# Kernel optimization log

Hardware: AMD Instinct MI355X
Metric: run time of the kernel (lower is better)

## Reference

```python
import jax, jax.numpy as jnp
import numpy as np

N = 50000
F_DIM = 128
H_DIM = 128
E = 800000


def setup_inputs() -> dict:
    key = jax.random.key(0)
    ks = jax.random.split(key, 8)
    x = jax.random.normal(ks[0], (N, F_DIM), dtype=jnp.float32)
    edge_weight = jax.random.uniform(ks[1], (E,), dtype=jnp.float32)
    src = jax.random.randint(ks[2], (E,), 0, N)
    dst = jax.random.randint(ks[3], (E,), 0, N)
    edge_index = jnp.stack([src, dst]).astype(jnp.int64)
    sc = 1.0 / np.sqrt(F_DIM)
    W1 = jax.random.normal(ks[4], (F_DIM, H_DIM), dtype=jnp.float32) * sc
    W2 = jax.random.normal(ks[5], (H_DIM, H_DIM), dtype=jnp.float32) * sc
    Wfc = jax.random.normal(ks[6], (H_DIM, F_DIM), dtype=jnp.float32) * sc
    b1 = jnp.zeros((H_DIM,), jnp.float32)
    b2 = jnp.zeros((H_DIM,), jnp.float32)
    bfc = jnp.zeros((F_DIM,), jnp.float32)
    return {"x": x, "edge_weight": edge_weight, "W1": W1, "b1": b1,
            "W2": W2, "b2": b2, "Wfc": Wfc, "bfc": bfc,
            "edge_index": edge_index}


def _gcn_norm(src, dst, edge_weight, num_nodes):
    # PyG gcn_norm: add self-loops (weight 1), symmetric D^-1/2 A D^-1/2
    loop = jnp.arange(num_nodes, dtype=src.dtype)
    src2 = jnp.concatenate([src, loop])
    dst2 = jnp.concatenate([dst, loop])
    w2 = jnp.concatenate([edge_weight, jnp.ones((num_nodes,), edge_weight.dtype)])
    deg = jax.ops.segment_sum(w2, dst2, num_segments=num_nodes)
    dinv = jnp.where(deg > 0, jax.lax.rsqrt(jnp.where(deg > 0, deg, 1.0)), 0.0)
    norm = dinv[src2] * w2 * dinv[dst2]
    return src2, dst2, norm


def _gcn_conv(x, W, b, src, dst, norm, num_nodes):
    h = x @ W                              # [N, out]
    msg = norm[:, None] * h[src]           # gather + scale, [E+N, out]
    agg = jax.ops.segment_sum(msg, dst, num_segments=num_nodes)
    return agg + b


def reference(x, edge_weight, W1, b1, W2, b2, Wfc, bfc, edge_index):
    src, dst = edge_index[0], edge_index[1]
    src2, dst2, norm = _gcn_norm(src, dst, edge_weight, N)
    h = jax.nn.relu(_gcn_conv(x, W1, b1, src2, dst2, norm, N))
    h = jax.nn.relu(_gcn_conv(h, W2, b2, src2, dst2, norm, N))
    return h @ Wfc + bfc
```

## Files before the change

kernel.cpp:

```cpp
#include <hip/hip_runtime.h>
#include <hip/hip_fp16.h>


typedef unsigned long long u64;
typedef _Float16 f16x8 __attribute__((ext_vector_type(8)));
typedef float f32x4 __attribute__((ext_vector_type(4)));

__global__ __launch_bounds__(256) void k_init(u64* packed, int n) {
    int i = blockIdx.x * 256 + threadIdx.x;
    if (i < n) packed[i] = 0ULL;
}

__global__ __launch_bounds__(256) void k_edge_deg(const int* __restrict__ dst,
                                                  const float* __restrict__ w,
                                                  u64* __restrict__ packed,
                                                  unsigned int* __restrict__ rank, int E) {
    int e = blockIdx.x * 256 + threadIdx.x;
    if (e < E) {
        int d = dst[e];
        u64 add = (1ULL << 40) | (u64)(w[e] * 16777216.0f);
        u64 old = atomicAdd(&packed[d], add);
        rank[e] = (unsigned int)(old >> 40);
    }
}

__global__ __launch_bounds__(256) void k_part(const u64* __restrict__ packed,
                                              float* __restrict__ dinv,
                                              int* __restrict__ bsum, int n) {
    __shared__ int red[256];
    int t = threadIdx.x;
    int i = blockIdx.x * 256 + t;
    int c = 0;
    if (i < n) {
        u64 p = packed[i];
        c = (int)(p >> 40);
        float degsum = (float)(p & ((1ULL << 40) - 1)) * (1.0f / 16777216.0f);
        dinv[i] = rsqrtf(1.0f + degsum);
    }
    red[t] = c;
    __syncthreads();
#pragma unroll
    for (int off = 128; off > 0; off >>= 1) {
        if (t < off) red[t] += red[t + off];
        __syncthreads();
    }
    if (t == 0) bsum[blockIdx.x] = red[0];
}

__global__ __launch_bounds__(256) void k_scan_bsums(int* bsum, int nb) {
    __shared__ int s[256];
    int t = threadIdx.x;
    s[t] = (t < nb) ? bsum[t] : 0;
    __syncthreads();
#pragma unroll
    for (int off = 1; off < 256; off <<= 1) {
        int u = (t >= off) ? s[t - off] : 0;
        __syncthreads();
        s[t] += u;
        __syncthreads();
    }
    if (t < nb) bsum[t] = (t == 0) ? 0 : s[t - 1];
}

__global__ __launch_bounds__(256) void k_rowptr(const u64* __restrict__ packed,
                                                const int* __restrict__ bsum,
                                                int* __restrict__ rowptr, int n) {
    __shared__ int s[256];
    int t = threadIdx.x;
    int i = blockIdx.x * 256 + t;
    int c = (i < n) ? (int)(packed[i] >> 40) : 0;
    s[t] = c;
    __syncthreads();
#pragma unroll
    for (int off = 1; off < 256; off <<= 1) {
        int u = (t >= off) ? s[t - off] : 0;
        __syncthreads();
        s[t] += u;
        __syncthreads();
    }
    int excl = bsum[blockIdx.x] + s[t] - c;
    if (i < n) rowptr[i] = excl;
    if (i == n - 1) rowptr[n] = excl + c;
}

__global__ __launch_bounds__(256) void k_scatter(const int* __restrict__ src,
                                                 const int* __restrict__ dst,
                                                 const float* __restrict__ w,
                                                 const unsigned int* __restrict__ rank,
                                                 const float* __restrict__ dinv,
                                                 const int* __restrict__ rowptr,
                                                 int* __restrict__ col,
                                                 float* __restrict__ val, int E) {
    int e = blockIdx.x * 256 + threadIdx.x;
    if (e < E) {
        int s = src[e], d = dst[e];
        int p = rowptr[d] + (int)rank[e];
        col[p] = s;
        val[p] = dinv[s] * w[e] * dinv[d];
    }
}

__global__ __launch_bounds__(256) void k_prepw(const float* __restrict__ W1,
                                               const float* __restrict__ W2,
                                               const float* __restrict__ Wfc,
                                               __half* __restrict__ Wt) {
    int i = blockIdx.x * 256 + threadIdx.x;
    if (i >= 3 * 16384) return;
    int w = i >> 14, r = i & 16383;
    int nn = r >> 7, kk = r & 127;
    const float* W = (w == 0) ? W1 : (w == 1) ? W2 : Wfc;
    Wt[i] = __float2half(W[kk * 128 + nn]);
}

template <bool IN_FP32, bool OUT_HALF>
__global__ __launch_bounds__(256) void k_gemm_mfma(const void* __restrict__ Xv,
                                                   const __half* __restrict__ Wt,
                                                   const float* __restrict__ bias,
                                                   void* __restrict__ Yv, int n) {
    __shared__ __align__(16) _Float16 Ws[128][136];
    int t = threadIdx.x;
    for (int i = t; i < 2048; i += 256) {
        int r = i >> 4, c8 = (i & 15) << 3;
        *(f16x8*)&Ws[r][c8] = *(const f16x8*)((const _Float16*)Wt + r * 128 + c8);
    }
    __syncthreads();

    int wave = t >> 6, lane = t & 63;
    int quad = lane >> 4, fcol = lane & 15;
    int rowbase = blockIdx.x * 64 + wave * 16;
    int arow = rowbase + fcol;

    f16x8 a[4];
#pragma unroll
    for (int c = 0; c < 4; c++) {
        int k0 = c * 32 + quad * 8;
        if (arow < n) {
            if (IN_FP32) {
                const float* p = (const float*)Xv + (size_t)arow * 128 + k0;
#pragma unroll
                for (int j = 0; j < 8; j++) a[c][j] = (_Float16)p[j];
            } else {
                a[c] = *(const f16x8*)((const _Float16*)Xv + (size_t)arow * 128 + k0);
            }
        } else {
            f16x8 z = {0, 0, 0, 0, 0, 0, 0, 0};
            a[c] = z;
        }
    }

    f32x4 acc[8];
#pragma unroll
    for (int c = 0; c < 8; c++) acc[c] = (f32x4){0.f, 0.f, 0.f, 0.f};

#pragma unroll
    for (int kc = 0; kc < 4; kc++) {
        int k0 = kc * 32 + quad * 8;
#pragma unroll
        for (int ct = 0; ct < 8; ct++) {
            f16x8 b = *(const f16x8*)&Ws[ct * 16 + fcol][k0];
            acc[ct] = __builtin_amdgcn_mfma_f32_16x16x32_f16(a[kc], b, acc[ct], 0, 0, 0);
        }
    }

#pragma unroll
    for (int reg = 0; reg < 4; reg++) {
        int gr = rowbase + quad * 4 + reg;
        if (gr < n) {
            if (OUT_HALF) {
                __half* Y = (__half*)Yv;
#pragma unroll
                for (int ct = 0; ct < 8; ct++)
                    Y[(size_t)gr * 128 + ct * 16 + fcol] = __float2half(acc[ct][reg]);
            } else {
                float* Y = (float*)Yv;
#pragma unroll
                for (int ct = 0; ct < 8; ct++)
                    Y[(size_t)gr * 128 + ct * 16 + fcol] = acc[ct][reg] + bias[ct * 16 + fcol];
            }
        }
    }
}

__global__ __launch_bounds__(256) void k_agg(const __half* __restrict__ H,
                                             const int* __restrict__ rowptr,
                                             const int* __restrict__ col,
                                             const float* __restrict__ val,
                                             const float* __restrict__ dinv,
                                             const float* __restrict__ bias,
                                             __half* __restrict__ out, int n) {
    int wid = (blockIdx.x * 256 + threadIdx.x) >> 6;
    int lane = threadIdx.x & 63;
    if (wid >= n) return;
    int i = __builtin_amdgcn_readfirstlane(wid);
    float di = dinv[i];
    float2 h0 = __half22float2(((const __half2*)(H + (size_t)i * 128))[lane]);
    float w0 = di * di;
    float ax = w0 * h0.x, ay = w0 * h0.y;
    int e0 = rowptr[i], e1 = rowptr[i + 1];

    for (int base = e0; base < e1; base += 64) {
        int cnt = min(64, e1 - base);
        int myc = 0; float myv = 0.f;
        if (lane < cnt) { myc = col[base + lane]; myv = val[base + lane]; }
        int j = 0;
        for (; j + 8 <= cnt; j += 8) {
            float2 h[8];
            float v[8];
#pragma unroll
            for (int u = 0; u < 8; u++) {
                int s = __shfl(myc, j + u);
                v[u] = __shfl(myv, j + u);
                h[u] = __half22float2(((const __half2*)(H + (size_t)s * 128))[lane]);
            }
#pragma unroll
            for (int u = 0; u < 8; u++) {
                ax = fmaf(v[u], h[u].x, ax);
                ay = fmaf(v[u], h[u].y, ay);
            }
        }
        for (; j < cnt; j++) {
            int s = __shfl(myc, j);
            float v = __shfl(myv, j);
            float2 h = __half22float2(((const __half2*)(H + (size_t)s * 128))[lane]);
            ax = fmaf(v, h.x, ax);
            ay = fmaf(v, h.y, ay);
        }
    }
    float2 b = ((const float2*)bias)[lane];
    ax = fmaxf(ax + b.x, 0.f);
    ay = fmaxf(ay + b.y, 0.f);
    ((__half2*)(out + (size_t)i * 128))[lane] = __floats2half2_rn(ax, ay);
}

extern "C" void kernel_launch(void* const* d_in, const int* in_sizes, int n_in,
                              void* d_out, int out_size, void* d_ws, size_t ws_size,
                              hipStream_t stream) {
    const float* x   = (const float*)d_in[0];
    const float* ew  = (const float*)d_in[1];
    const float* W1  = (const float*)d_in[2];
    const float* b1  = (const float*)d_in[3];
    const float* W2  = (const float*)d_in[4];
    const float* b2  = (const float*)d_in[5];
    const float* Wfc = (const float*)d_in[6];
    const float* bfc = (const float*)d_in[7];
    const int* eidx  = (const int*)d_in[8];

    const int E = in_sizes[1];
    const int N = in_sizes[0] / 128;
    const int* src = eidx;
    const int* dst = eidx + E;

    char* ws = (char*)d_ws;
    size_t off = 0;
    auto alloc = [&](size_t bytes) -> void* {
        void* p = ws + off;
        off = (off + bytes + 255) & ~(size_t)255;
        return p;
    };
    int nb = (N + 255) / 256;
    int eb = (E + 255) / 256;
    int gb = (N + 63) / 64;
    int ab = (N * 64 + 255) / 256;
    int Npad = N + 64;

    u64*   packed = (u64*)alloc((size_t)N * 8);
    float* dinv   = (float*)alloc((size_t)N * 4);
    int*   rowptr = (int*)alloc((size_t)(N + 1) * 4);
    int*   bsum   = (int*)alloc((size_t)nb * 4);
    unsigned int* rank = (unsigned int*)alloc((size_t)E * 4);
    int*   col    = (int*)alloc((size_t)E * 4);
    float* val    = (float*)alloc((size_t)E * 4);
    __half* Wt    = (__half*)alloc((size_t)3 * 16384 * 2);
    __half* bufH  = (__half*)alloc((size_t)Npad * 128 * 2);
    __half* bufA  = (__half*)alloc((size_t)Npad * 128 * 2);

    k_init<<<nb, 256, 0, stream>>>(packed, N);
    k_edge_deg<<<eb, 256, 0, stream>>>(dst, ew, packed, rank, E);
    k_part<<<nb, 256, 0, stream>>>(packed, dinv, bsum, N);
    k_scan_bsums<<<1, 256, 0, stream>>>(bsum, nb);
    k_rowptr<<<nb, 256, 0, stream>>>(packed, bsum, rowptr, N);
    k_scatter<<<eb, 256, 0, stream>>>(src, dst, ew, rank, dinv, rowptr, col, val, E);
    k_prepw<<<192, 256, 0, stream>>>(W1, W2, Wfc, Wt);

    k_gemm_mfma<true, true><<<gb, 256, 0, stream>>>(x, Wt, nullptr, bufH, N);
    k_agg<<<ab, 256, 0, stream>>>(bufH, rowptr, col, val, dinv, b1, bufA, N);
    k_gemm_mfma<false, true><<<gb, 256, 0, stream>>>(bufA, Wt + 16384, nullptr, bufH, N);
    k_agg<<<ab, 256, 0, stream>>>(bufH, rowptr, col, val, dinv, b2, bufA, N);
    k_gemm_mfma<false, false><<<gb, 256, 0, stream>>>(bufA, Wt + 2 * 16384, bfc, d_out, N);
}
```

Measured before the change: 259.0 us.

## Fuse setup kernels, co-launch degree with first GEMM, pack CSR pairs

Merges the init and weight-prep kernels into one launch. The degree-atomic pass and the first GEMM now share a single grid, so independent work runs concurrently. The separate col/val arrays become one int2 pairs array, so k_agg does one load per edge, and its inner gather loop is unrolled to 16 with a masked 8-wide tail. The GEMM reads weights straight from global memory instead of staging them in LDS, which drops the barrier but may add L1/L2 traffic.

```diff
diff --git a/kernel.cpp b/kernel.cpp
--- a/kernel.cpp
+++ b/kernel.cpp
@@ -6,22 +6,110 @@
 typedef _Float16 f16x8 __attribute__((ext_vector_type(8)));
 typedef float f32x4 __attribute__((ext_vector_type(4)));
 
-__global__ __launch_bounds__(256) void k_init(u64* packed, int n) {
+__global__ __launch_bounds__(256) void k_pre(u64* packed, int n,
+                                             const float* __restrict__ W1,
+                                             const float* __restrict__ W2,
+                                             const float* __restrict__ Wfc,
+                                             __half* __restrict__ Wt) {
     int i = blockIdx.x * 256 + threadIdx.x;
     if (i < n) packed[i] = 0ULL;
-}
-
-__global__ __launch_bounds__(256) void k_edge_deg(const int* __restrict__ dst,
-                                                  const float* __restrict__ w,
-                                                  u64* __restrict__ packed,
-                                                  unsigned int* __restrict__ rank, int E) {
-    int e = blockIdx.x * 256 + threadIdx.x;
-    if (e < E) {
-        int d = dst[e];
-        u64 add = (1ULL << 40) | (u64)(w[e] * 16777216.0f);
-        u64 old = atomicAdd(&packed[d], add);
-        rank[e] = (unsigned int)(old >> 40);
-    }
+    if (i < 3 * 16384) {
+        int w = i >> 14, r = i & 16383;
+        int nn = r >> 7, kk = r & 127;
+        const float* W = (w == 0) ? W1 : (w == 1) ? W2 : Wfc;
+        Wt[i] = __float2half(W[kk * 128 + nn]);
+    }
+}
+
+template <bool IN_FP32, bool OUT_HALF>
+__device__ __forceinline__ void gemm_body(int bid, int t, const void* __restrict__ Xv,
+                                          const _Float16* __restrict__ Wt,
+                                          const float* __restrict__ bias,
+                                          void* __restrict__ Yv, int n) {
+    int wave = t >> 6, lane = t & 63;
+    int quad = lane >> 4, fcol = lane & 15;
+    int rowbase = bid * 64 + wave * 16;
+    int arow = rowbase + fcol;
+
+    f16x8 a[4];
+#pragma unroll
+    for (int c = 0; c < 4; c++) {
+        int k0 = c * 32 + quad * 8;
+        if (arow < n) {
+            if (IN_FP32) {
+                const float* p = (const float*)Xv + (size_t)arow * 128 + k0;
+#pragma unroll
+                for (int j = 0; j < 8; j++) a[c][j] = (_Float16)p[j];
+            } else {
+                a[c] = *(const f16x8*)((const _Float16*)Xv + (size_t)arow * 128 + k0);
+            }
+        } else {
+            f16x8 z = {0, 0, 0, 0, 0, 0, 0, 0};
+            a[c] = z;
+        }
+    }
+
+    f32x4 acc[8];
+#pragma unroll
+    for (int c = 0; c < 8; c++) acc[c] = (f32x4){0.f, 0.f, 0.f, 0.f};
+
+#pragma unroll
+    for (int kc = 0; kc < 4; kc++) {
+        int k0 = kc * 32 + quad * 8;
+#pragma unroll
+        for (int ct = 0; ct < 8; ct++) {
+            f16x8 b = *(const f16x8*)(Wt + (size_t)(ct * 16 + fcol) * 128 + k0);
+            acc[ct] = __builtin_amdgcn_mfma_f32_16x16x32_f16(a[kc], b, acc[ct], 0, 0, 0);
+        }
+    }
+
+#pragma unroll
+    for (int reg = 0; reg < 4; reg++) {
+        int gr = rowbase + quad * 4 + reg;
+        if (gr < n) {
+            if (OUT_HALF) {
+                __half* Y = (__half*)Yv;
+#pragma unroll
+                for (int ct = 0; ct < 8; ct++)
+                    Y[(size_t)gr * 128 + ct * 16 + fcol] = __float2half(acc[ct][reg]);
+            } else {
+                float* Y = (float*)Yv;
+#pragma unroll
+                for (int ct = 0; ct < 8; ct++)
+                    Y[(size_t)gr * 128 + ct * 16 + fcol] = acc[ct][reg] + bias[ct * 16 + fcol];
+            }
+        }
+    }
+}
+
+__global__ __launch_bounds__(256) void k_deg_gemm1(const int* __restrict__ dst,
+                                                   const float* __restrict__ ew,
+                                                   u64* __restrict__ packed,
+                                                   unsigned int* __restrict__ rank,
+                                                   int E, int eb,
+                                                   const float* __restrict__ x,
+                                                   const _Float16* __restrict__ Wt,
+                                                   __half* __restrict__ bufH, int n) {
+    int t = threadIdx.x;
+    if ((int)blockIdx.x < eb) {
+        int e = blockIdx.x * 256 + t;
+        if (e < E) {
+            int d = dst[e];
+            u64 add = (1ULL << 40) | (u64)(ew[e] * 16777216.0f);
+            u64 old = atomicAdd(&packed[d], add);
+            rank[e] = (unsigned int)(old >> 40);
+        }
+    } else {
+        gemm_body<true, true>(blockIdx.x - eb, t, x, Wt, nullptr, bufH, n);
+    }
+}
+
+template <bool IN_FP32, bool OUT_HALF>
+__global__ __launch_bounds__(256) void k_gemm(const void* __restrict__ Xv,
+                                              const _Float16* __restrict__ Wt,
+                                              const float* __restrict__ bias,
+                                              void* __restrict__ Yv, int n) {
+    gemm_body<IN_FP32, OUT_HALF>(blockIdx.x, threadIdx.x, Xv, Wt, bias, Yv, n);
 }
 
 __global__ __launch_bounds__(256) void k_part(const u64* __restrict__ packed,
@@ -89,102 +177,18 @@
                                                  const unsigned int* __restrict__ rank,
                                                  const float* __restrict__ dinv,
                                                  const int* __restrict__ rowptr,
-                                                 int* __restrict__ col,
-                                                 float* __restrict__ val, int E) {
+                                                 int2* __restrict__ pairs, int E) {
     int e = blockIdx.x * 256 + threadIdx.x;
     if (e < E) {
         int s = src[e], d = dst[e];
         int p = rowptr[d] + (int)rank[e];
-        col[p] = s;
-        val[p] = dinv[s] * w[e] * dinv[d];
-    }
-}
-
-__global__ __launch_bounds__(256) void k_prepw(const float* __restrict__ W1,
-                                               const float* __restrict__ W2,
-                                               const float* __restrict__ Wfc,
-                                               __half* __restrict__ Wt) {
-    int i = blockIdx.x * 256 + threadIdx.x;
-    if (i >= 3 * 16384) return;
-    int w = i >> 14, r = i & 16383;
-    int nn = r >> 7, kk = r & 127;
-    const float* W = (w == 0) ? W1 : (w == 1) ? W2 : Wfc;
-    Wt[i] = __float2half(W[kk * 128 + nn]);
-}
-
-template <bool IN_FP32, bool OUT_HALF>
-__global__ __launch_bounds__(256) void k_gemm_mfma(const void* __restrict__ Xv,
-                                                   const __half* __restrict__ Wt,
-                                                   const float* __restrict__ bias,
-                                                   void* __restrict__ Yv, int n) {
-    __shared__ __align__(16) _Float16 Ws[128][136];
-    int t = threadIdx.x;
-    for (int i = t; i < 2048; i += 256) {
-        int r = i >> 4, c8 = (i & 15) << 3;
-        *(f16x8*)&Ws[r][c8] = *(const f16x8*)((const _Float16*)Wt + r * 128 + c8);
-    }
-    __syncthreads();
-
-    int wave = t >> 6, lane = t & 63;
-    int quad = lane >> 4, fcol = lane & 15;
-    int rowbase = blockIdx.x * 64 + wave * 16;
-    int arow = rowbase + fcol;
-
-    f16x8 a[4];
-#pragma unroll
-    for (int c = 0; c < 4; c++) {
-        int k0 = c * 32 + quad * 8;
-        if (arow < n) {
-            if (IN_FP32) {
-                const float* p = (const float*)Xv + (size_t)arow * 128 + k0;
-#pragma unroll
-                for (int j = 0; j < 8; j++) a[c][j] = (_Float16)p[j];
-            } else {
-                a[c] = *(const f16x8*)((const _Float16*)Xv + (size_t)arow * 128 + k0);
-            }
-        } else {
-            f16x8 z = {0, 0, 0, 0, 0, 0, 0, 0};
-            a[c] = z;
-        }
-    }
-
-    f32x4 acc[8];
-#pragma unroll
-    for (int c = 0; c < 8; c++) acc[c] = (f32x4){0.f, 0.f, 0.f, 0.f};
-
-#pragma unroll
-    for (int kc = 0; kc < 4; kc++) {
-        int k0 = kc * 32 + quad * 8;
-#pragma unroll
-        for (int ct = 0; ct < 8; ct++) {
-            f16x8 b = *(const f16x8*)&Ws[ct * 16 + fcol][k0];
-            acc[ct] = __builtin_amdgcn_mfma_f32_16x16x32_f16(a[kc], b, acc[ct], 0, 0, 0);
-        }
-    }
-
-#pragma unroll
-    for (int reg = 0; reg < 4; reg++) {
-        int gr = rowbase + quad * 4 + reg;
-        if (gr < n) {
-            if (OUT_HALF) {
-                __half* Y = (__half*)Yv;
-#pragma unroll
-                for (int ct = 0; ct < 8; ct++)
-                    Y[(size_t)gr * 128 + ct * 16 + fcol] = __float2half(acc[ct][reg]);
-            } else {
-                float* Y = (float*)Yv;
-#pragma unroll
-                for (int ct = 0; ct < 8; ct++)
-                    Y[(size_t)gr * 128 + ct * 16 + fcol] = acc[ct][reg] + bias[ct * 16 + fcol];
-            }
-        }
+        pairs[p] = make_int2(s, __float_as_int(dinv[s] * w[e] * dinv[d]));
     }
 }
 
 __global__ __launch_bounds__(256) void k_agg(const __half* __restrict__ H,
                                              const int* __restrict__ rowptr,
-                                             const int* __restrict__ col,
-                                             const float* __restrict__ val,
+                                             const int2* __restrict__ pairs,
                                              const float* __restrict__ dinv,
                                              const float* __restrict__ bias,
                                              __half* __restrict__ out, int n) {
@@ -200,16 +204,38 @@
 
     for (int base = e0; base < e1; base += 64) {
         int cnt = min(64, e1 - base);
-        int myc = 0; float myv = 0.f;
-        if (lane < cnt) { myc = col[base + lane]; myv = val[base + lane]; }
+        int mys = 0; float myv = 0.f;
+        if (lane < cnt) {
+            int2 pr = pairs[base + lane];
+            mys = pr.x;
+            myv = __int_as_float(pr.y);
+        }
         int j = 0;
-        for (; j + 8 <= cnt; j += 8) {
+        for (; j + 16 <= cnt; j += 16) {
+            float2 h[16];
+            float v[16];
+#pragma unroll
+            for (int u = 0; u < 16; u++) {
+                int s = __shfl(mys, j + u);
+                v[u] = __shfl(myv, j + u);
+                h[u] = __half22float2(((const __half2*)(H + (size_t)s * 128))[lane]);
+            }
+#pragma unroll
+            for (int u = 0; u < 16; u++) {
+                ax = fmaf(v[u], h[u].x, ax);
+                ay = fmaf(v[u], h[u].y, ay);
+            }
+        }
+        for (; j < cnt; j += 8) {
             float2 h[8];
             float v[8];
 #pragma unroll
             for (int u = 0; u < 8; u++) {
-                int s = __shfl(myc, j + u);
-                v[u] = __shfl(myv, j + u);
+                int idx = j + u;
+                int lsrc = min(idx, cnt - 1);
+                int s = __shfl(mys, lsrc);
+                float tv = __shfl(myv, lsrc);
+                v[u] = (idx < cnt) ? tv : 0.f;
                 h[u] = __half22float2(((const __half2*)(H + (size_t)s * 128))[lane]);
             }
 #pragma unroll
@@ -217,13 +243,6 @@
                 ax = fmaf(v[u], h[u].x, ax);
                 ay = fmaf(v[u], h[u].y, ay);
             }
-        }
-        for (; j < cnt; j++) {
-            int s = __shfl(myc, j);
-            float v = __shfl(myv, j);
-            float2 h = __half22float2(((const __half2*)(H + (size_t)s * 128))[lane]);
-            ax = fmaf(v, h.x, ax);
-            ay = fmaf(v, h.y, ay);
         }
     }
     float2 b = ((const float2*)bias)[lane];
@@ -261,6 +280,7 @@
     int eb = (E + 255) / 256;
     int gb = (N + 63) / 64;
     int ab = (N * 64 + 255) / 256;
+    int pb = (max(N, 3 * 16384) + 255) / 256;
     int Npad = N + 64;
 
     u64*   packed = (u64*)alloc((size_t)N * 8);
@@ -268,23 +288,25 @@
     int*   rowptr = (int*)alloc((size_t)(N + 1) * 4);
     int*   bsum   = (int*)alloc((size_t)nb * 4);
     unsigned int* rank = (unsigned int*)alloc((size_t)E * 4);
-    int*   col    = (int*)alloc((size_t)E * 4);
-    float* val    = (float*)alloc((size_t)E * 4);
+    int2*  pairs  = (int2*)alloc((size_t)E * 8);
     __half* Wt    = (__half*)alloc((size_t)3 * 16384 * 2);
     __half* bufH  = (__half*)alloc((size_t)Npad * 128 * 2);
     __half* bufA  = (__half*)alloc((size_t)Npad * 128 * 2);
 
-    k_init<<<nb, 256, 0, stream>>>(packed, N);
-    k_edge_deg<<<eb, 256, 0, stream>>>(dst, ew, packed, rank, E);
+    const _Float16* Wt1 = (const _Float16*)Wt;
+    const _Float16* Wt2 = Wt1 + 16384;
+    const _Float16* Wt3 = Wt1 + 2 * 16384;
+
+    k_pre<<<pb, 256, 0, stream>>>(packed, N, W1, W2, Wfc, Wt);
+    k_deg_gemm1<<<eb + gb, 256, 0, stream>>>(dst, ew, packed, rank, E, eb,
+                                             x, Wt1, bufH, N);
     k_part<<<nb, 256, 0, stream>>>(packed, dinv, bsum, N);
     k_scan_bsums<<<1, 256, 0, stream>>>(bsum, nb);
     k_rowptr<<<nb, 256, 0, stream>>>(packed, bsum, rowptr, N);
-    k_scatter<<<eb, 256, 0, stream>>>(src, dst, ew, rank, dinv, rowptr, col, val, E);
-    k_prepw<<<192, 256, 0, stream>>>(W1, W2, Wfc, Wt);
-
-    k_gemm_mfma<true, true><<<gb, 256, 0, stream>>>(x, Wt, nullptr, bufH, N);
-    k_agg<<<ab, 256, 0, stream>>>(bufH, rowptr, col, val, dinv, b1, bufA, N);
-    k_gemm_mfma<false, true><<<gb, 256, 0, stream>>>(bufA, Wt + 16384, nullptr, bufH, N);
-    k_agg<<<ab, 256, 0, stream>>>(bufH, rowptr, col, val, dinv, b2, bufA, N);
-    k_gemm_mfma<false, false><<<gb, 256, 0, stream>>>(bufA, Wt + 2 * 16384, bfc, d_out, N);
-}
+    k_scatter<<<eb, 256, 0, stream>>>(src, dst, ew, rank, dinv, rowptr, pairs, E);
+
+    k_agg<<<ab, 256, 0, stream>>>(bufH, rowptr, pairs, dinv, b1, bufA, N);
+    k_gemm<false, true><<<gb, 256, 0, stream>>>(bufA, Wt2, nullptr, bufH, N);
+    k_agg<<<ab, 256, 0, stream>>>(bufH, rowptr, pairs, dinv, b2, bufA, N);
+    k_gemm<false, false><<<gb, 256, 0, stream>>>(bufA, Wt3, bfc, d_out, N);
+}
```

Measured after the change: 279.8 us. 8.0% more time.
